# Optimization experiments

Hardware: AMD Instinct MI355X
Metric: run time of the kernel (lower is better)

The kernel has to match this reference:

```python
import jax, jax.numpy as jnp
import numpy as np

WINDOW = 16
VD = 6
HID = 16


def setup_inputs() -> dict:
    key = jax.random.key(0)
    ks = jax.random.split(key, 10)
    B, S = 256, 4096
    sc = 0.1
    return {
        "x": jax.random.normal(ks[0], (B, S, 2), jnp.float32),
        "h_0": jnp.zeros((B, HID), jnp.float32),
        "fir_I_w": jax.random.normal(ks[1], (VD, WINDOW), jnp.float32) * sc,
        "fir_Q_w": jax.random.normal(ks[2], (VD, WINDOW), jnp.float32) * sc,
        "W_fi_w": jax.random.normal(ks[3], (HID, 2 * VD), jnp.float32) * sc,
        "W_fi_b": jnp.zeros((HID,), jnp.float32),
        "W_fh_w": jax.random.normal(ks[4], (HID, HID), jnp.float32) * sc,
        "W_gi_w": jax.random.normal(ks[5], (HID, 2 * VD), jnp.float32) * sc,
        "W_gi_b": jnp.zeros((HID,), jnp.float32),
        "W_gh_w": jax.random.normal(ks[6], (HID, HID), jnp.float32) * sc,
        "W_out_I_w": jax.random.normal(ks[7], (1, HID), jnp.float32) * sc,
        "W_out_I_b": jnp.zeros((1,), jnp.float32),
        "W_out_Q_w": jax.random.normal(ks[8], (1, HID), jnp.float32) * sc,
        "W_out_Q_b": jnp.zeros((1,), jnp.float32),
    }


def _tile_theta(t, hidden):
    # pr_block replication logic for vd_units < hidden <= 3*vd_units cases
    if VD >= hidden:
        return t[..., :hidden]
    elif hidden <= 2 * VD:
        return jnp.concatenate([t, t[..., : hidden - VD]], axis=-1)
    else:
        return jnp.concatenate([t, t, t[..., : hidden - 2 * VD]], axis=-1)


def reference(x, h_0, fir_I_w, fir_Q_w, W_fi_w, W_fi_b, W_fh_w,
              W_gi_w, W_gi_b, W_gh_w, W_out_I_w, W_out_I_b,
              W_out_Q_w, W_out_Q_b):
    B, S, _ = x.shape
    # Causal sliding windows: window at t covers x[t-15 .. t] with zero pad.
    xp = jnp.concatenate([jnp.zeros((B, WINDOW - 1, 2), x.dtype), x], axis=1)
    idx = jnp.arange(S)[:, None] + jnp.arange(WINDOW)[None, :]  # (S, W)
    win = xp[:, idx, :]  # (B, S, W, 2)
    wI, wQ = win[..., 0], win[..., 1]  # (B, S, W)
    # Complex FIR filter
    I_fir = jnp.einsum('bsw,vw->bsv', wI, fir_I_w) - jnp.einsum('bsw,vw->bsv', wQ, fir_Q_w)
    Q_fir = jnp.einsum('bsw,vw->bsv', wI, fir_Q_w) + jnp.einsum('bsw,vw->bsv', wQ, fir_I_w)
    mag = jnp.sqrt(I_fir * I_fir + Q_fir * Q_fir) + 1e-8
    mag2 = mag * mag
    sin_t = Q_fir / mag
    cos_t = I_fir / mag
    # L = stack([mag, mag2], dim=2).view(B, S, 2*VD)
    L = jnp.stack([mag, mag2], axis=2).reshape(B, S, 2 * VD)
    # Precompute input contributions to gates; scan the recurrence.
    fi = jnp.einsum('bsl,hl->bsh', L, W_fi_w) + W_fi_b  # (B,S,H)
    gi = jnp.einsum('bsl,hl->bsh', L, W_gi_w) + W_gi_b

    def step(h, inp):
        fi_t, gi_t = inp
        f = jax.nn.sigmoid(fi_t + h @ W_fh_w.T)
        g = jnp.tanh(gi_t + h @ W_gh_w.T)
        h = f * h + (1.0 - f) * g
        return h, h

    _, h_seq = jax.lax.scan(step, h_0, (fi.transpose(1, 0, 2), gi.transpose(1, 0, 2)))
    h_seq = h_seq.transpose(1, 0, 2)  # (B, S, H)
    hidden = h_seq.shape[-1]
    cos_r = _tile_theta(cos_t, hidden)
    sin_r = _tile_theta(sin_t, hidden)
    I_rot = h_seq * cos_r
    Q_rot = h_seq * sin_r
    oI = I_rot @ W_out_I_w.T + W_out_I_b  # (B,S,1)
    oQ = Q_rot @ W_out_Q_w.T + W_out_Q_b
    out_I = oI - oQ
    out_Q = oQ + oI
    return jnp.concatenate([out_I, out_Q], axis=-1)
```

## Files before the change

kernel.cpp:

```cpp
#include <hip/hip_runtime.h>
#include <stdint.h>

#define DEV __device__ __forceinline__

constexpr int Bb   = 256;
constexpr int Ss   = 4096;
constexpr int HIDN = 16;
constexpr int VDN  = 6;
constexpr int WINN = 16;

constexpr int BPG   = 32;
constexpr int NG    = Bb / BPG;
constexpr int CHUNK = 16;
constexpr int WARM  = 16;
constexpr int NCH   = Ss / CHUNK;
constexpr int NPH   = (CHUNK + WARM) / 4;
constexpr int EPH   = WARM / 4;

constexpr size_t WSL_BYTES = (size_t)NG * Ss * 64 * 16;
constexpr size_t WSC_BYTES = (size_t)NG * Ss * BPG * 24;

typedef __fp16 h2v  __attribute__((ext_vector_type(2)));
typedef __fp16 f16x8 __attribute__((ext_vector_type(8)));
typedef float  f32x16 __attribute__((ext_vector_type(16)));

DEV uint32_t pk16(float a, float b) {
    h2v t = __builtin_amdgcn_cvt_pkrtz(a, b);
    uint32_t u; __builtin_memcpy(&u, &t, 4); return u;
}
DEV void up16(uint32_t u, float& a, float& b) {
    h2v t; __builtin_memcpy(&t, &u, 4);
    a = (float)t[0]; b = (float)t[1];
}
DEV f32x16 MF(const uint32_t* a, const uint32_t* b, f32x16 c) {
    f16x8 av, bv;
    __builtin_memcpy(&av, a, 16);
    __builtin_memcpy(&bv, b, 16);
    return __builtin_amdgcn_mfma_f32_32x32x16_f16(av, bv, c, 0, 0, 0);
}

template<int C> DEV int   dpp_i(int v)  { return __builtin_amdgcn_update_dpp(0, v, C, 0xF, 0xF, false); }
template<int C> DEV float dpp_f(float v){ return __int_as_float(dpp_i<C>(__float_as_int(v))); }
#define DPP_ALL(X) X(1,0x121) X(2,0x122) X(3,0x123) X(4,0x124) X(5,0x125) X(6,0x126) X(7,0x127) \
  X(8,0x128) X(9,0x129) X(10,0x12A) X(11,0x12B) X(12,0x12C) X(13,0x12D) X(14,0x12E) X(15,0x12F)

__global__ __launch_bounds__(256, 4) void boja_front(
    const float* __restrict__ x,
    const float* __restrict__ fIw, const float* __restrict__ fQw,
    uint4* __restrict__ wsl, uint2* __restrict__ wsc)
{
    __shared__ __align__(16) uint32_t lds[8 * 64 * 4];
    const int tid = threadIdx.x;
    const int tq  = tid & 7;
    const int b_  = tid >> 3;
    const int G   = blockIdx.y;
    const int t0  = blockIdx.x * 8;
    const int t   = t0 + tq;
    const int b   = G * BPG + b_;
    const int id  = b * Ss + t;
    const float2* x2 = (const float2*)x;

    float wI[WINN], wQ[WINN];
    if (t >= WINN - 1) {
#pragma unroll
        for (int w = 0; w < WINN; ++w) { float2 v = x2[id - 15 + w]; wI[w] = v.x; wQ[w] = v.y; }
    } else {
#pragma unroll
        for (int w = 0; w < WINN; ++w) {
            int ts = t - 15 + w;
            float2 v = (ts >= 0) ? x2[id - 15 + w] : make_float2(0.f, 0.f);
            wI[w] = v.x; wQ[w] = v.y;
        }
    }
    float aI[VDN], aQ[VDN];
#pragma unroll
    for (int v = 0; v < VDN; ++v) { aI[v] = 0.f; aQ[v] = 0.f; }
#pragma unroll
    for (int w = 0; w < WINN; ++w) {
#pragma unroll
        for (int v = 0; v < VDN; ++v) {
            aI[v] = fmaf( wI[w], fIw[v*16+w], aI[v]);
            aI[v] = fmaf(-wQ[w], fQw[v*16+w], aI[v]);
            aQ[v] = fmaf( wI[w], fQw[v*16+w], aQ[v]);
            aQ[v] = fmaf( wQ[w], fIw[v*16+w], aQ[v]);
        }
    }
    float L[12];
    uint32_t sc[6];
#pragma unroll
    for (int v = 0; v < VDN; ++v) {
        float m2 = fmaf(aI[v], aI[v], aQ[v]*aQ[v]);
        float mg = __builtin_amdgcn_sqrtf(m2) + 1e-8f;
        float iv = __builtin_amdgcn_rcpf(mg);
        L[v] = mg; L[6+v] = mg*mg;
        sc[v] = pk16(aI[v]*iv, aQ[v]*iv);
    }
    {
        const size_t cb = ((size_t)(G * Ss + t) * BPG + b_) * 3;
        wsc[cb+0] = make_uint2(sc[0], sc[1]);
        wsc[cb+1] = make_uint2(sc[2], sc[3]);
        wsc[cb+2] = make_uint2(sc[4], sc[5]);
    }
    const int lo = (tq*64 + b_) * 4, hi = (tq*64 + b_ + 32) * 4;
    lds[lo+0] = pk16(L[0], L[1]);  lds[lo+1] = pk16(L[2],  L[3]);
    lds[lo+2] = pk16(L[8], L[9]);  lds[lo+3] = pk16(L[10], L[11]);
    lds[hi+0] = pk16(L[4], L[5]);  lds[hi+1] = pk16(L[6],  L[7]);
    lds[hi+2] = 0x00003C00u;
    lds[hi+3] = 0u;
    __syncthreads();
#pragma unroll
    for (int r = 0; r < 2; ++r) {
        int idx = r*256 + tid;
        int tq2 = idx >> 6, lane = idx & 63;
        uint4 v = *(const uint4*)&lds[(tq2*64 + lane)*4];
        wsl[(size_t)(G*Ss + t0 + tq2) * 64 + lane] = v;
    }
}

__global__ __launch_bounds__(64, 2) void boja_rnn(
    const uint4* __restrict__ wsl, const uint2* __restrict__ wsc,
    const float* __restrict__ h0,
    const float* __restrict__ Wfh, const float* __restrict__ Wgh,
    const float* __restrict__ Wfi, const float* __restrict__ bfi,
    const float* __restrict__ Wgi, const float* __restrict__ bgi,
    const float* __restrict__ WoI, const float* __restrict__ boI,
    const float* __restrict__ WoQ, const float* __restrict__ boQ,
    float* __restrict__ out)
{
    const int l  = threadIdx.x;
    const int b_ = l & 31;
    const int h_ = l >> 5;
    const int G  = blockIdx.x & (NG - 1);
    const int ci = blockIdx.x >> 3;

    const int t_out0  = ci * CHUNK;
    const int t_start = t_out0 - WARM;
    const bool useh0  = (t_start <= 0);

    const float CF = -1.4426950408889634f;
    const float CG =  2.8853900817779268f;
    const int   m  = b_;
    const float sA = (m < 16) ? CF : CG;

    uint32_t a1[4], a2[4];
#pragma unroll
    for (int d = 0; d < 4; ++d) {
        float wv[2], uv[2];
#pragma unroll
        for (int q = 0; q < 2; ++q) {
            const int e = d*2 + q;
            const int k = (e & 3) + 8*(e >> 2) + 4*h_;
            wv[q] = ((m < 16) ? Wfh[m*16 + k] : Wgh[(m-16)*16 + k]) * sA;
            float u;
            if (k < 12)       u = ((m < 16) ? Wfi[m*12 + k] : Wgi[(m-16)*12 + k]) * sA;
            else if (k == 12) u = ((m < 16) ? bfi[m] : bgi[m-16]) * sA;
            else              u = 0.0f;
            uv[q] = u;
        }
        a1[d] = pk16(wv[0], wv[1]);
        a2[d] = pk16(uv[0], uv[1]);
    }

    float woi[8], woq[8];
#pragma unroll
    for (int r = 0; r < 8; ++r) {
        const int j = (r & 3) + 8*(r >> 2) + 4*h_;
        woi[r] = WoI[j]; woq[r] = WoQ[j];
    }
    const float bo_i = boI[0], bo_q = boQ[0];

    float h0r[8];
    if (useh0) {
        const float* hp = h0 + (size_t)(G*BPG + b_) * HIDN;
        float4 p = *(const float4*)(hp + 4*h_);
        float4 q = *(const float4*)(hp + 8 + 4*h_);
        h0r[0]=p.x; h0r[1]=p.y; h0r[2]=p.z; h0r[3]=p.w;
        h0r[4]=q.x; h0r[5]=q.y; h0r[6]=q.z; h0r[7]=q.w;
    }
    float hreg[8];
#pragma unroll
    for (int r = 0; r < 8; ++r) hreg[r] = 0.0f;
    uint32_t b1[4];
    b1[0]=0u; b1[1]=0u; b1[2]=0u; b1[3]=0u;

    f32x16 zero16;
#pragma unroll
    for (int i = 0; i < 16; ++i) zero16[i] = 0.0f;

    const uint4* lp = wsl + (size_t)G * Ss * 64 + l;
    const uint2* cp = wsc + ((size_t)G * Ss * BPG + b_) * 3;
    float2* outp = (float2*)out + (size_t)(G*BPG + b_) * Ss;

    uint4 LB[3][4];
    uint2 CB[2][4][3];

    auto loadL = [&](uint4 (&B)[4], int tb) {
#pragma unroll
        for (int s = 0; s < 4; ++s) {
            int tq2 = tb + s; tq2 = (tq2 < 0) ? 0 : tq2;
            B[s] = lp[(size_t)tq2 * 64];
        }
    };
    auto loadC = [&](uint2 (&C)[4][3], int tb) {
#pragma unroll
        for (int s = 0; s < 4; ++s)
#pragma unroll
            for (int k = 0; k < 3; ++k)
                C[s][k] = cp[(size_t)(tb + s) * (BPG*3) + k];
    };

    loadL(LB[0], t_start);
    loadL(LB[1], t_start + 4);

#define PHASE(P) { \
    const int tb = t_start + 4*(P); \
    if ((P) + 2 < NPH) loadL(LB[((P)+2)%3], t_start + 4*((P)+2)); \
    if ((P) + 1 >= EPH && (P) + 1 < NPH) loadC(CB[((P)+1)&1], t_start + 4*((P)+1)); \
    f32x16 accL = MF(a2, (const uint32_t*)&LB[(P)%3][0], zero16); \
    float ob[8]; \
    _Pragma("unroll") \
    for (int s = 0; s < 4; ++s) { \
        if (useh0 && tb + s == 0) { \
            _Pragma("unroll") for (int r = 0; r < 8; ++r) hreg[r] = h0r[r]; \
            b1[0]=pk16(hreg[0],hreg[1]); b1[1]=pk16(hreg[2],hreg[3]); \
            b1[2]=pk16(hreg[4],hreg[5]); b1[3]=pk16(hreg[6],hreg[7]); \
        } \
        f32x16 acc = MF(a1, b1, accL); \
        if (s < 3) accL = MF(a2, (const uint32_t*)&LB[(P)%3][s+1], zero16); \
        _Pragma("unroll") \
        for (int r = 0; r < 8; ++r) { \
            float f = __builtin_amdgcn_rcpf(1.0f + __builtin_amdgcn_exp2f(acc[r])); \
            float g = fmaf(-2.0f, __builtin_amdgcn_rcpf(1.0f + __builtin_amdgcn_exp2f(acc[r+8])), 1.0f); \
            hreg[r] = fmaf(f, hreg[r] - g, g); \
        } \
        b1[0]=pk16(hreg[0],hreg[1]); b1[1]=pk16(hreg[2],hreg[3]); \
        b1[2]=pk16(hreg[4],hreg[5]); b1[3]=pk16(hreg[6],hreg[7]); \
        if ((P) >= EPH) { \
            float cs6[6], sn6[6]; \
            up16(CB[(P)&1][s][0].x, cs6[0], sn6[0]); up16(CB[(P)&1][s][0].y, cs6[1], sn6[1]); \
            up16(CB[(P)&1][s][1].x, cs6[2], sn6[2]); up16(CB[(P)&1][s][1].y, cs6[3], sn6[3]); \
            up16(CB[(P)&1][s][2].x, cs6[4], sn6[4]); up16(CB[(P)&1][s][2].y, cs6[5], sn6[5]); \
            float oI = bo_i, oQ = bo_q; \
            const bool hb = (h_ != 0); \
            { \
                float c0,sn0; \
                c0 = hb?cs6[4]:cs6[0]; sn0 = hb?sn6[4]:sn6[0]; oI = fmaf(hreg[0]*c0, woi[0], oI); oQ = fmaf(hreg[0]*sn0, woq[0], oQ); \
                c0 = hb?cs6[5]:cs6[1]; sn0 = hb?sn6[5]:sn6[1]; oI = fmaf(hreg[1]*c0, woi[1], oI); oQ = fmaf(hreg[1]*sn0, woq[1], oQ); \
                c0 = hb?cs6[0]:cs6[2]; sn0 = hb?sn6[0]:sn6[2]; oI = fmaf(hreg[2]*c0, woi[2], oI); oQ = fmaf(hreg[2]*sn0, woq[2], oQ); \
                c0 = hb?cs6[1]:cs6[3]; sn0 = hb?sn6[1]:sn6[3]; oI = fmaf(hreg[3]*c0, woi[3], oI); oQ = fmaf(hreg[3]*sn0, woq[3], oQ); \
                c0 = hb?cs6[0]:cs6[2]; sn0 = hb?sn6[0]:sn6[2]; oI = fmaf(hreg[4]*c0, woi[4], oI); oQ = fmaf(hreg[4]*sn0, woq[4], oQ); \
                c0 = hb?cs6[1]:cs6[3]; sn0 = hb?sn6[1]:sn6[3]; oI = fmaf(hreg[5]*c0, woi[5], oI); oQ = fmaf(hreg[5]*sn0, woq[5], oQ); \
                c0 = hb?cs6[2]:cs6[4]; sn0 = hb?sn6[2]:sn6[4]; oI = fmaf(hreg[6]*c0, woi[6], oI); oQ = fmaf(hreg[6]*sn0, woq[6], oQ); \
                c0 = hb?cs6[3]:cs6[5]; sn0 = hb?sn6[3]:sn6[5]; oI = fmaf(hreg[7]*c0, woi[7], oI); oQ = fmaf(hreg[7]*sn0, woq[7], oQ); \
            } \
            oI += __shfl_xor(oI, 32, 64); \
            oQ += __shfl_xor(oQ, 32, 64); \
            ob[s*2] = oI - oQ; ob[s*2+1] = oI + oQ; \
        } \
    } \
    if ((P) >= EPH && l < 32) { \
        float4* po = (float4*)(outp + tb); \
        po[0] = make_float4(ob[0], ob[1], ob[2], ob[3]); \
        po[1] = make_float4(ob[4], ob[5], ob[6], ob[7]); \
    } \
}

    PHASE(0)  PHASE(1)  PHASE(2)  PHASE(3)
    PHASE(4)  PHASE(5)  PHASE(6)  PHASE(7)
#undef PHASE
}

__global__ __launch_bounds__(64, 2) void bojanet_v2(
    const float* __restrict__ x,   const float* __restrict__ h0,
    const float* __restrict__ fIw, const float* __restrict__ fQw,
    const float* __restrict__ Wfi, const float* __restrict__ bfi,
    const float* __restrict__ Wfh, const float* __restrict__ Wgi,
    const float* __restrict__ bgi, const float* __restrict__ Wgh,
    const float* __restrict__ WoI, const float* __restrict__ boI,
    const float* __restrict__ WoQ, const float* __restrict__ boQ,
    float* __restrict__ out)
{
    constexpr int FCH = 128, FWR = 64, FSB = 16;
    __shared__ __align__(16) float s_fi[FSB * 80];
    __shared__ __align__(16) float s_gi[FSB * 80];
    __shared__ __align__(16) float s_h [FSB * 68];
    __shared__ float s_sc[4 * 12 * 17];

    const int lane = threadIdx.x;
    const int j  = lane & 15;
    const int bl = lane >> 4;
    const int ci = blockIdx.x;
    const int b0 = blockIdx.y * 4;
    const int t_out0  = ci * FCH;
    const int t_start = ci ? (t_out0 - FWR) : 0;
    const int t_end   = t_out0 + FCH;

    int c[16]; c[0] = j;
#define CSET(K,CTL) c[K] = dpp_i<CTL>(j);
    DPP_ALL(CSET)
#undef CSET
    float wf[16], wg[16];
#pragma unroll
    for (int k = 0; k < 16; ++k) { wf[k] = Wfh[j*16 + c[k]]; wg[k] = Wgh[j*16 + c[k]]; }

    float h = (ci == 0) ? h0[(b0 + bl) * HIDN + j] : 0.0f;
    const float2* x2   = (const float2*)x + (size_t)(b0 + bl) * Ss;
    float2*       out2 = (float2*)out     + (size_t)(b0 + bl) * Ss;

    for (int tb = t_start; tb < t_end; tb += FSB) {
        const bool emit = (tb >= t_out0);
        {
            const int tg = tb + j;
            float wI[WINN], wQ[WINN];
            if (tb >= WINN - 1) {
#pragma unroll
                for (int w = 0; w < WINN; ++w) { float2 v = x2[tg - 15 + w]; wI[w] = v.x; wQ[w] = v.y; }
            } else {
#pragma unroll
                for (int w = 0; w < WINN; ++w) {
                    int ts = tg - 15 + w;
                    float2 v = (ts >= 0) ? x2[ts] : make_float2(0.f, 0.f);
                    wI[w] = v.x; wQ[w] = v.y;
                }
            }
            float aI[VDN], aQ[VDN];
#pragma unroll
            for (int v = 0; v < VDN; ++v) { aI[v] = 0.f; aQ[v] = 0.f; }
#pragma unroll
            for (int w = 0; w < WINN; ++w) {
#pragma unroll
                for (int v = 0; v < VDN; ++v) {
                    aI[v] = fmaf( wI[w], fIw[v*16+w], aI[v]);
                    aI[v] = fmaf(-wQ[w], fQw[v*16+w], aI[v]);
                    aQ[v] = fmaf( wI[w], fQw[v*16+w], aQ[v]);
                    aQ[v] = fmaf( wQ[w], fIw[v*16+w], aQ[v]);
                }
            }
            float L[12];
#pragma unroll
            for (int v = 0; v < VDN; ++v) {
                float m2 = fmaf(aI[v], aI[v], aQ[v]*aQ[v]);
                float mg = __builtin_amdgcn_sqrtf(m2) + 1e-8f;
                L[v] = mg; L[6+v] = mg*mg;
                if (emit) {
                    float iv = __builtin_amdgcn_rcpf(mg);
                    s_sc[(bl*12 + v  )*17 + j] = aI[v] * iv;
                    s_sc[(bl*12 + 6+v)*17 + j] = aQ[v] * iv;
                }
            }
            float fi[16], gi[16];
#pragma unroll
            for (int k = 0; k < 16; ++k) { fi[k] = bfi[k]; gi[k] = bgi[k]; }
#pragma unroll
            for (int ll = 0; ll < 12; ++ll) {
#pragma unroll
                for (int k = 0; k < 16; ++k) {
                    fi[k] = fmaf(L[ll], Wfi[k*12+ll], fi[k]);
                    gi[k] = fmaf(L[ll], Wgi[k*12+ll], gi[k]);
                }
            }
            float* pf = &s_fi[j*80 + bl*20];
            float* pg = &s_gi[j*80 + bl*20];
#pragma unroll
            for (int qq = 0; qq < 4; ++qq) {
                *(float4*)(pf + 4*qq) = make_float4(fi[4*qq], fi[4*qq+1], fi[4*qq+2], fi[4*qq+3]);
                *(float4*)(pg + 4*qq) = make_float4(gi[4*qq], gi[4*qq+1], gi[4*qq+2], gi[4*qq+3]);
            }
        }
        __asm__ volatile("s_waitcnt lgkmcnt(0)" ::: "memory");
        {
            const int rb = bl*20 + j;
            float pf0 = s_fi[rb], pf1 = s_fi[80 + rb];
            float pg0 = s_gi[rb], pg1 = s_gi[80 + rb];
#pragma unroll
            for (int tt = 0; tt < FSB; ++tt) {
                const int nx = (tt + 2 < FSB) ? tt + 2 : FSB - 1;
                float pfn = s_fi[nx*80 + rb];
                float pgn = s_gi[nx*80 + rb];
                float hr[16]; hr[0] = h;
#define HSET(K,CTL) hr[K] = dpp_f<CTL>(h);
                DPP_ALL(HSET)
#undef HSET
                float af0 = pf0, af1 = 0.f, ag0 = pg0, ag1 = 0.f;
#pragma unroll
                for (int k = 0; k < 8; ++k) {
                    af0 = fmaf(wf[k],   hr[k],   af0);
                    ag0 = fmaf(wg[k],   hr[k],   ag0);
                    af1 = fmaf(wf[k+8], hr[k+8], af1);
                    ag1 = fmaf(wg[k+8], hr[k+8], ag1);
                }
                float zf = af0 + af1, zg = ag0 + ag1;
                float f = __builtin_amdgcn_rcpf(1.0f + __builtin_amdgcn_exp2f(zf * -1.4426950408889634f));
                float g = fmaf(-2.0f, __builtin_amdgcn_rcpf(1.0f + __builtin_amdgcn_exp2f(zg * 2.8853900817779268f)), 1.0f);
                h = fmaf(f, h - g, g);
                s_h[tt*68 + bl*16 + j] = h;
                pf0 = pf1; pf1 = pfn; pg0 = pg1; pg1 = pgn;
            }
        }
        __asm__ volatile("s_waitcnt lgkmcnt(0)" ::: "memory");
        if (emit) {
            const int tg = tb + j;
            float hv[16];
#pragma unroll
            for (int qq = 0; qq < 4; ++qq) {
                float4 t4 = *(const float4*)&s_h[j*68 + bl*16 + 4*qq];
                hv[4*qq] = t4.x; hv[4*qq+1] = t4.y; hv[4*qq+2] = t4.z; hv[4*qq+3] = t4.w;
            }
            float cs[12];
#pragma unroll
            for (int k = 0; k < 12; ++k) cs[k] = s_sc[(bl*12 + k)*17 + j];
            float oI = boI[0], oQ = boQ[0];
#pragma unroll
            for (int k = 0; k < 16; ++k) {
                int v = (k < 6) ? k : ((k < 12) ? k - 6 : k - 12);
                oI = fmaf(hv[k]*cs[v],   WoI[k], oI);
                oQ = fmaf(hv[k]*cs[6+v], WoQ[k], oQ);
            }
            out2[tg] = make_float2(oI - oQ, oI + oQ);
        }
        __asm__ volatile("s_waitcnt lgkmcnt(0)" ::: "memory");
    }
}

extern "C" void kernel_launch(void* const* d_in, const int* in_sizes, int n_in,
                              void* d_out, int out_size, void* d_ws, size_t ws_size,
                              hipStream_t stream) {
    const float* x   = (const float*)d_in[0];
    const float* h0  = (const float*)d_in[1];
    const float* fIw = (const float*)d_in[2];
    const float* fQw = (const float*)d_in[3];
    const float* Wfi = (const float*)d_in[4];
    const float* bfi = (const float*)d_in[5];
    const float* Wfh = (const float*)d_in[6];
    const float* Wgi = (const float*)d_in[7];
    const float* bgi = (const float*)d_in[8];
    const float* Wgh = (const float*)d_in[9];
    const float* WoI = (const float*)d_in[10];
    const float* boI = (const float*)d_in[11];
    const float* WoQ = (const float*)d_in[12];
    const float* boQ = (const float*)d_in[13];
    float* out = (float*)d_out;

    if (ws_size >= WSL_BYTES + WSC_BYTES) {
        uint4* wsl = (uint4*)d_ws;
        uint2* wsc = (uint2*)((char*)d_ws + WSL_BYTES);
        boja_front<<<dim3(Ss/8, NG), 256, 0, stream>>>(x, fIw, fQw, wsl, wsc);
        boja_rnn<<<dim3(NG * NCH), 64, 0, stream>>>(
            wsl, wsc, h0, Wfh, Wgh, Wfi, bfi, Wgi, bgi, WoI, boI, WoQ, boQ, out);
    } else {
        bojanet_v2<<<dim3(32, Bb / 4), 64, 0, stream>>>(
            x, h0, fIw, fQw, Wfi, bfi, Wfh, Wgi, bgi, Wgh, WoI, boI, WoQ, boQ, out);
    }
}
```

Baseline: 49.52 us.

## Split RNN output projection into separate kernel and halve recurrence chunk size

The recurrence kernel no longer computes the rotated output projection. It writes fp16 hidden states to a new workspace buffer, and a third kernel, boja_out, reads h together with the stored cos/sin values, computes the outputs, and writes them through LDS in a coalesced layout. With that work gone, CHUNK drops from 16 to 8, which doubles the number of chunk blocks, and launch bounds rise to 4 waves, so parallelism goes up and per-block latency goes down. The costs are a larger share of redundant warmup steps per chunk, extra global traffic for the hidden-state round trip, an added launch, and h now being rounded to fp16 before the output projection.

```diff
diff --git a/kernel.cpp b/kernel.cpp
--- a/kernel.cpp
+++ b/kernel.cpp
@@ -11,7 +11,7 @@
 
 constexpr int BPG   = 32;
 constexpr int NG    = Bb / BPG;
-constexpr int CHUNK = 16;
+constexpr int CHUNK = 8;
 constexpr int WARM  = 16;
 constexpr int NCH   = Ss / CHUNK;
 constexpr int NPH   = (CHUNK + WARM) / 4;
@@ -19,6 +19,7 @@
 
 constexpr size_t WSL_BYTES = (size_t)NG * Ss * 64 * 16;
 constexpr size_t WSC_BYTES = (size_t)NG * Ss * BPG * 24;
+constexpr size_t HWS_BYTES = (size_t)NG * Ss * BPG * 32;
 
 typedef __fp16 h2v  __attribute__((ext_vector_type(2)));
 typedef __fp16 f16x8 __attribute__((ext_vector_type(8)));
@@ -117,15 +118,12 @@
     }
 }
 
-__global__ __launch_bounds__(64, 2) void boja_rnn(
-    const uint4* __restrict__ wsl, const uint2* __restrict__ wsc,
-    const float* __restrict__ h0,
+__global__ __launch_bounds__(64, 4) void boja_rnn(
+    const uint4* __restrict__ wsl, const float* __restrict__ h0,
     const float* __restrict__ Wfh, const float* __restrict__ Wgh,
     const float* __restrict__ Wfi, const float* __restrict__ bfi,
     const float* __restrict__ Wgi, const float* __restrict__ bgi,
-    const float* __restrict__ WoI, const float* __restrict__ boI,
-    const float* __restrict__ WoQ, const float* __restrict__ boQ,
-    float* __restrict__ out)
+    uint4* __restrict__ hws)
 {
     const int l  = threadIdx.x;
     const int b_ = l & 31;
@@ -161,22 +159,6 @@
         a2[d] = pk16(uv[0], uv[1]);
     }
 
-    float woi[8], woq[8];
-#pragma unroll
-    for (int r = 0; r < 8; ++r) {
-        const int j = (r & 3) + 8*(r >> 2) + 4*h_;
-        woi[r] = WoI[j]; woq[r] = WoQ[j];
-    }
-    const float bo_i = boI[0], bo_q = boQ[0];
-
-    float h0r[8];
-    if (useh0) {
-        const float* hp = h0 + (size_t)(G*BPG + b_) * HIDN;
-        float4 p = *(const float4*)(hp + 4*h_);
-        float4 q = *(const float4*)(hp + 8 + 4*h_);
-        h0r[0]=p.x; h0r[1]=p.y; h0r[2]=p.z; h0r[3]=p.w;
-        h0r[4]=q.x; h0r[5]=q.y; h0r[6]=q.z; h0r[7]=q.w;
-    }
     float hreg[8];
 #pragma unroll
     for (int r = 0; r < 8; ++r) hreg[r] = 0.0f;
@@ -188,12 +170,9 @@
     for (int i = 0; i < 16; ++i) zero16[i] = 0.0f;
 
     const uint4* lp = wsl + (size_t)G * Ss * 64 + l;
-    const uint2* cp = wsc + ((size_t)G * Ss * BPG + b_) * 3;
-    float2* outp = (float2*)out + (size_t)(G*BPG + b_) * Ss;
+    uint4* hwp = hws + ((size_t)G * Ss) * 64;
 
     uint4 LB[3][4];
-    uint2 CB[2][4][3];
-
     auto loadL = [&](uint4 (&B)[4], int tb) {
 #pragma unroll
         for (int s = 0; s < 4; ++s) {
@@ -201,13 +180,6 @@
             B[s] = lp[(size_t)tq2 * 64];
         }
     };
-    auto loadC = [&](uint2 (&C)[4][3], int tb) {
-#pragma unroll
-        for (int s = 0; s < 4; ++s)
-#pragma unroll
-            for (int k = 0; k < 3; ++k)
-                C[s][k] = cp[(size_t)(tb + s) * (BPG*3) + k];
-    };
 
     loadL(LB[0], t_start);
     loadL(LB[1], t_start + 4);
@@ -215,18 +187,19 @@
 #define PHASE(P) { \
     const int tb = t_start + 4*(P); \
     if ((P) + 2 < NPH) loadL(LB[((P)+2)%3], t_start + 4*((P)+2)); \
-    if ((P) + 1 >= EPH && (P) + 1 < NPH) loadC(CB[((P)+1)&1], t_start + 4*((P)+1)); \
-    f32x16 accL = MF(a2, (const uint32_t*)&LB[(P)%3][0], zero16); \
-    float ob[8]; \
+    if (useh0 && tb == 0) { \
+        const float* hp = h0 + (size_t)(G*BPG + b_) * HIDN; \
+        float4 p = *(const float4*)(hp + 4*h_); \
+        float4 q = *(const float4*)(hp + 8 + 4*h_); \
+        hreg[0]=p.x; hreg[1]=p.y; hreg[2]=p.z; hreg[3]=p.w; \
+        hreg[4]=q.x; hreg[5]=q.y; hreg[6]=q.z; hreg[7]=q.w; \
+        b1[0]=pk16(hreg[0],hreg[1]); b1[1]=pk16(hreg[2],hreg[3]); \
+        b1[2]=pk16(hreg[4],hreg[5]); b1[3]=pk16(hreg[6],hreg[7]); \
+    } \
     _Pragma("unroll") \
     for (int s = 0; s < 4; ++s) { \
-        if (useh0 && tb + s == 0) { \
-            _Pragma("unroll") for (int r = 0; r < 8; ++r) hreg[r] = h0r[r]; \
-            b1[0]=pk16(hreg[0],hreg[1]); b1[1]=pk16(hreg[2],hreg[3]); \
-            b1[2]=pk16(hreg[4],hreg[5]); b1[3]=pk16(hreg[6],hreg[7]); \
-        } \
-        f32x16 acc = MF(a1, b1, accL); \
-        if (s < 3) accL = MF(a2, (const uint32_t*)&LB[(P)%3][s+1], zero16); \
+        f32x16 acc = MF(a1, b1, zero16); \
+        acc = MF(a2, (const uint32_t*)&LB[(P)%3][s], acc); \
         _Pragma("unroll") \
         for (int r = 0; r < 8; ++r) { \
             float f = __builtin_amdgcn_rcpf(1.0f + __builtin_amdgcn_exp2f(acc[r])); \
@@ -236,38 +209,62 @@
         b1[0]=pk16(hreg[0],hreg[1]); b1[1]=pk16(hreg[2],hreg[3]); \
         b1[2]=pk16(hreg[4],hreg[5]); b1[3]=pk16(hreg[6],hreg[7]); \
         if ((P) >= EPH) { \
-            float cs6[6], sn6[6]; \
-            up16(CB[(P)&1][s][0].x, cs6[0], sn6[0]); up16(CB[(P)&1][s][0].y, cs6[1], sn6[1]); \
-            up16(CB[(P)&1][s][1].x, cs6[2], sn6[2]); up16(CB[(P)&1][s][1].y, cs6[3], sn6[3]); \
-            up16(CB[(P)&1][s][2].x, cs6[4], sn6[4]); up16(CB[(P)&1][s][2].y, cs6[5], sn6[5]); \
-            float oI = bo_i, oQ = bo_q; \
-            const bool hb = (h_ != 0); \
-            { \
-                float c0,sn0; \
-                c0 = hb?cs6[4]:cs6[0]; sn0 = hb?sn6[4]:sn6[0]; oI = fmaf(hreg[0]*c0, woi[0], oI); oQ = fmaf(hreg[0]*sn0, woq[0], oQ); \
-                c0 = hb?cs6[5]:cs6[1]; sn0 = hb?sn6[5]:sn6[1]; oI = fmaf(hreg[1]*c0, woi[1], oI); oQ = fmaf(hreg[1]*sn0, woq[1], oQ); \
-                c0 = hb?cs6[0]:cs6[2]; sn0 = hb?sn6[0]:sn6[2]; oI = fmaf(hreg[2]*c0, woi[2], oI); oQ = fmaf(hreg[2]*sn0, woq[2], oQ); \
-                c0 = hb?cs6[1]:cs6[3]; sn0 = hb?sn6[1]:sn6[3]; oI = fmaf(hreg[3]*c0, woi[3], oI); oQ = fmaf(hreg[3]*sn0, woq[3], oQ); \
-                c0 = hb?cs6[0]:cs6[2]; sn0 = hb?sn6[0]:sn6[2]; oI = fmaf(hreg[4]*c0, woi[4], oI); oQ = fmaf(hreg[4]*sn0, woq[4], oQ); \
-                c0 = hb?cs6[1]:cs6[3]; sn0 = hb?sn6[1]:sn6[3]; oI = fmaf(hreg[5]*c0, woi[5], oI); oQ = fmaf(hreg[5]*sn0, woq[5], oQ); \
-                c0 = hb?cs6[2]:cs6[4]; sn0 = hb?sn6[2]:sn6[4]; oI = fmaf(hreg[6]*c0, woi[6], oI); oQ = fmaf(hreg[6]*sn0, woq[6], oQ); \
-                c0 = hb?cs6[3]:cs6[5]; sn0 = hb?sn6[3]:sn6[5]; oI = fmaf(hreg[7]*c0, woi[7], oI); oQ = fmaf(hreg[7]*sn0, woq[7], oQ); \
-            } \
-            oI += __shfl_xor(oI, 32, 64); \
-            oQ += __shfl_xor(oQ, 32, 64); \
-            ob[s*2] = oI - oQ; ob[s*2+1] = oI + oQ; \
+            hwp[((size_t)(tb + s) * 32 + b_) * 2 + h_] = \
+                make_uint4(b1[0], b1[1], b1[2], b1[3]); \
         } \
     } \
-    if ((P) >= EPH && l < 32) { \
-        float4* po = (float4*)(outp + tb); \
-        po[0] = make_float4(ob[0], ob[1], ob[2], ob[3]); \
-        po[1] = make_float4(ob[4], ob[5], ob[6], ob[7]); \
-    } \
-}
-
-    PHASE(0)  PHASE(1)  PHASE(2)  PHASE(3)
-    PHASE(4)  PHASE(5)  PHASE(6)  PHASE(7)
+}
+
+    PHASE(0)  PHASE(1)  PHASE(2)
+    PHASE(3)  PHASE(4)  PHASE(5)
 #undef PHASE
+}
+
+__global__ __launch_bounds__(256, 4) void boja_out(
+    const uint4* __restrict__ hws, const uint2* __restrict__ wsc,
+    const float* __restrict__ WoI, const float* __restrict__ boI,
+    const float* __restrict__ WoQ, const float* __restrict__ boQ,
+    float* __restrict__ out)
+{
+    __shared__ float2 s_out[8 * 33];
+
+    const int tid = threadIdx.x;
+    const int b   = tid & 31;
+    const int tl  = tid >> 5;
+    const int G   = blockIdx.y;
+    const int t0  = blockIdx.x * 8;
+    const int t   = t0 + tl;
+    const size_t item = (size_t)G * Ss + t;
+    const size_t base = item * 32 + b;
+
+    uint4 hw0 = hws[base*2];
+    uint4 hw1 = hws[base*2 + 1];
+    const uint2* cp = wsc + base*3;
+    uint2 r0 = cp[0], r1 = cp[1], r2 = cp[2];
+
+    float hv[16];
+    up16(hw0.x, hv[0],  hv[1]);  up16(hw0.y, hv[2],  hv[3]);
+    up16(hw0.z, hv[8],  hv[9]);  up16(hw0.w, hv[10], hv[11]);
+    up16(hw1.x, hv[4],  hv[5]);  up16(hw1.y, hv[6],  hv[7]);
+    up16(hw1.z, hv[12], hv[13]); up16(hw1.w, hv[14], hv[15]);
+
+    float cv[6], sv[6];
+    up16(r0.x, cv[0], sv[0]); up16(r0.y, cv[1], sv[1]);
+    up16(r1.x, cv[2], sv[2]); up16(r1.y, cv[3], sv[3]);
+    up16(r2.x, cv[4], sv[4]); up16(r2.y, cv[5], sv[5]);
+
+    float oI = boI[0], oQ = boQ[0];
+#pragma unroll
+    for (int j = 0; j < 16; ++j) {
+        const int v = (j < 6) ? j : ((j < 12) ? j - 6 : j - 12);
+        oI = fmaf(hv[j]*cv[v], WoI[j], oI);
+        oQ = fmaf(hv[j]*sv[v], WoQ[j], oQ);
+    }
+    s_out[tl*33 + b] = make_float2(oI - oQ, oI + oQ);
+    __syncthreads();
+
+    const int b2 = tid >> 3, tl2 = tid & 7;
+    ((float2*)out)[(size_t)(G*BPG + b2) * Ss + t0 + tl2] = s_out[tl2*33 + b2];
 }
 
 __global__ __launch_bounds__(64, 2) void bojanet_v2(
@@ -441,12 +438,15 @@
     const float* boQ = (const float*)d_in[13];
     float* out = (float*)d_out;
 
-    if (ws_size >= WSL_BYTES + WSC_BYTES) {
+    if (ws_size >= WSL_BYTES + WSC_BYTES + HWS_BYTES) {
         uint4* wsl = (uint4*)d_ws;
         uint2* wsc = (uint2*)((char*)d_ws + WSL_BYTES);
+        uint4* hws = (uint4*)((char*)d_ws + WSL_BYTES + WSC_BYTES);
         boja_front<<<dim3(Ss/8, NG), 256, 0, stream>>>(x, fIw, fQw, wsl, wsc);
         boja_rnn<<<dim3(NG * NCH), 64, 0, stream>>>(
-            wsl, wsc, h0, Wfh, Wgh, Wfi, bfi, Wgi, bgi, WoI, boI, WoQ, boQ, out);
+            wsl, h0, Wfh, Wgh, Wfi, bfi, Wgi, bgi, hws);
+        boja_out<<<dim3(Ss/8, NG), 256, 0, stream>>>(
+            hws, wsc, WoI, boI, WoQ, boQ, out);
     } else {
         bojanet_v2<<<dim3(32, Bb / 4), 64, 0, stream>>>(
             x, h0, fIw, fQw, Wfi, bfi, Wfh, Wgi, bgi, Wgh, WoI, boI, WoQ, boQ, out);
```

Measured after the change: 66.56 us. +34.4%, slower.
